# Kernel tuning notes

Hardware: AMD Instinct MI355X
Metric: run time of the kernel (lower is better)

The kernel has to match this reference:

```python
import jax, jax.numpy as jnp
import numpy as np

B, S, D, H = 8, 1024, 1024, 16
DK = D // H  # 64


def setup_inputs() -> dict:
    key = jax.random.key(0)
    ks = jax.random.split(key, 12)
    def w(k):
        return (jax.random.normal(k, (D, D), dtype=jnp.float32) * 0.02)
    def b(k):
        return (jax.random.normal(k, (D,), dtype=jnp.float32) * 0.02)
    return {
        "q": jax.random.normal(ks[0], (B, S, D), dtype=jnp.float32),
        "k": jax.random.normal(ks[1], (B, S, D), dtype=jnp.float32),
        "v": jax.random.normal(ks[2], (B, S, D), dtype=jnp.float32),
        "mask": jax.random.randint(ks[3], (B, 1, S, S), 0, 2, dtype=jnp.int32),
        "WQ_w": w(ks[4]), "WQ_b": b(ks[5]),
        "WK_w": w(ks[6]), "WK_b": b(ks[7]),
        "WV_w": w(ks[8]), "WV_b": b(ks[9]),
        "WO_w": w(ks[10]), "WO_b": b(ks[11]),
    }


def reference(q, k, v, mask, WQ_w, WQ_b, WK_w, WK_b, WV_w, WV_b, WO_w, WO_b):
    # nn.Linear: y = x @ W.T + b
    Q = (q @ WQ_w.T + WQ_b).reshape(B, S, H, DK)
    K = (k @ WK_w.T + WK_b).reshape(B, S, H, DK)
    V = (v @ WV_w.T + WV_b).reshape(B, S, H, DK)
    # scores: [B, H, Sq, Sk]
    scores = jnp.einsum("bqhd,bkhd->bhqk", Q, K) / jnp.sqrt(jnp.float32(DK))
    scores = jnp.where(mask == 0, jnp.float32(-1e9), scores)
    attn = jax.nn.softmax(scores, axis=-1)
    # dropout p=0.0 -> identity
    out = jnp.einsum("bhqk,bkhd->bqhd", attn, V).reshape(B, S, D)
    return out @ WO_w.T + WO_b
```

## Files before the change

kernel.cpp:

```cpp
#include <hip/hip_runtime.h>
#include <math.h>

typedef __bf16 bf16;
typedef __bf16 bf16x8 __attribute__((ext_vector_type(8)));
typedef __bf16 bf16x4 __attribute__((ext_vector_type(4)));
typedef float f32x4 __attribute__((ext_vector_type(4)));

constexpr int B_ = 8, S_ = 1024, D_ = 1024, H_ = 16, DK_ = 64;
constexpr int M_ = B_ * S_;
constexpr size_t A8 = (size_t)1 << 23;
constexpr size_t W1 = (size_t)1 << 20;
constexpr float QSCALE = 0.18033688011112042f;

#if __has_builtin(__builtin_amdgcn_exp2f)
#define EXP2F(x) __builtin_amdgcn_exp2f(x)
#else
#define EXP2F(x) exp2f(x)
#endif
#if __has_builtin(__builtin_amdgcn_rcpf)
#define RCPF(x) __builtin_amdgcn_rcpf(x)
#else
#define RCPF(x) (1.0f / (x))
#endif

#define GAS(p) ((const __attribute__((address_space(1))) void*)(p))
#define LAS(p) ((__attribute__((address_space(3))) void*)(p))

template<int CTRL>
__device__ __forceinline__ float row_ror(float v) {
    int i = __builtin_bit_cast(int, v);
    i = __builtin_amdgcn_update_dpp(i, i, CTRL, 0xF, 0xF, false);
    return __builtin_bit_cast(float, i);
}
__device__ __forceinline__ float rowmax16(float v) {
    v = fmaxf(v, row_ror<0x121>(v));
    v = fmaxf(v, row_ror<0x122>(v));
    v = fmaxf(v, row_ror<0x124>(v));
    v = fmaxf(v, row_ror<0x128>(v));
    return v;
}
__device__ __forceinline__ float rowsum16(float v) {
    v += row_ror<0x121>(v);
    v += row_ror<0x122>(v);
    v += row_ror<0x124>(v);
    v += row_ror<0x128>(v);
    return v;
}

__global__ __launch_bounds__(256) void cvt_all(
    const float* __restrict__ q, const float* __restrict__ k,
    const float* __restrict__ v, const float* __restrict__ w0,
    const float* __restrict__ w1, const float* __restrict__ w2,
    const float* __restrict__ w3, bf16* __restrict__ dst)
{
    size_t e = ((size_t)blockIdx.x * 256 + threadIdx.x) * 8;
    const float* src;
    size_t off;
    if (e < 3 * A8) {
        int t = (int)(e >> 23);
        src = (t == 0) ? q : (t == 1) ? k : v;
        off = e & (A8 - 1);
    } else {
        size_t ew = e - 3 * A8;
        int t = (int)(ew >> 20);
        src = (t == 0) ? w0 : (t == 1) ? w1 : (t == 2) ? w2 : w3;
        off = ew & (W1 - 1);
    }
    float4 a = *(const float4*)(src + off);
    float4 b = *(const float4*)(src + off + 4);
    bf16x8 o = { (bf16)a.x, (bf16)a.y, (bf16)a.z, (bf16)a.w,
                 (bf16)b.x, (bf16)b.y, (bf16)b.z, (bf16)b.w };
    *(bf16x8*)(dst + e) = o;
}

__global__ __launch_bounds__(256) void mask_cvt(
    const int* __restrict__ mask, bf16* __restrict__ mp)
{
    const int bx = blockIdx.x;
    const int kt = bx & 15, qt = (bx >> 4) & 15, b = bx >> 8;
    const int tid = threadIdx.x;
    const int w = tid >> 6, lane = tid & 63;
    const int quad = lane >> 4, l15 = lane & 15;

    const int* src = mask + ((size_t)b << 20)
                   + (size_t)(qt * 64 + w * 16 + quad * 4) * 1024
                   + kt * 64 + l15;
    bf16 vals[16];
#pragma unroll
    for (int j = 0; j < 4; ++j)
#pragma unroll
        for (int r = 0; r < 4; ++r) {
            int m = src[(size_t)r * 1024 + j * 16];
            vals[j * 4 + r] = m ? (bf16)0.0f : (bf16)(-1e9f);
        }
    bf16* dst = mp + (((size_t)(b * 16 + qt) * 16 + kt) << 12) + (w * 64 + lane) * 16;
    bf16x8 o0 = { vals[0], vals[1], vals[2],  vals[3],  vals[4],  vals[5],  vals[6],  vals[7]  };
    bf16x8 o1 = { vals[8], vals[9], vals[10], vals[11], vals[12], vals[13], vals[14], vals[15] };
    *(bf16x8*)dst = o0;
    *(bf16x8*)(dst + 8) = o1;
}

template<int OUT_MODE>
__global__ __launch_bounds__(256) void gemm_mfma(
    const bf16* __restrict__ X, const bf16* __restrict__ W,
    const float* __restrict__ bias, void* __restrict__ outv, float oscale)
{
    constexpr int K = 1024;
    __shared__ bf16 As[128 * 32];
    __shared__ bf16 Bs[128 * 32];

    const int tid  = threadIdx.x;
    const int lane = tid & 63;
    const int w    = tid >> 6;
    const int wm   = w & 1, wn = w >> 1;
    const int quad = lane >> 4, l15 = lane & 15;
    const int bm = blockIdx.x * 128, bn = blockIdx.y * 128;

    f32x4 acc[4][4];
#pragma unroll
    for (int i = 0; i < 4; ++i)
#pragma unroll
        for (int j = 0; j < 4; ++j)
#pragma unroll
            for (int r = 0; r < 4; ++r) acc[i][j][r] = 0.f;

    const int lrow = lane >> 2;
    const int lcol = (lane & 3) * 8;

    for (int k0 = 0; k0 < K; k0 += 32) {
        __syncthreads();
#pragma unroll
        for (int i = 0; i < 2; ++i) {
            const int rbase = w * 16 + i * 64;
            __builtin_amdgcn_global_load_lds(
                GAS(X + (size_t)(bm + rbase + lrow) * K + k0 + lcol),
                LAS(As + rbase * 32), 16, 0, 0);
            __builtin_amdgcn_global_load_lds(
                GAS(W + (size_t)(bn + rbase + lrow) * K + k0 + lcol),
                LAS(Bs + rbase * 32), 16, 0, 0);
        }
        __syncthreads();

        bf16x8 a[4], b[4];
#pragma unroll
        for (int i = 0; i < 4; ++i)
            a[i] = *(const bf16x8*)(As + (wm * 64 + i * 16 + l15) * 32 + quad * 8);
#pragma unroll
        for (int j = 0; j < 4; ++j)
            b[j] = *(const bf16x8*)(Bs + (wn * 64 + j * 16 + l15) * 32 + quad * 8);
#pragma unroll
        for (int i = 0; i < 4; ++i)
#pragma unroll
            for (int j = 0; j < 4; ++j)
                acc[i][j] = __builtin_amdgcn_mfma_f32_16x16x32_bf16(
                    a[i], b[j], acc[i][j], 0, 0, 0);
    }

#pragma unroll
    for (int i = 0; i < 4; ++i) {
#pragma unroll
        for (int j = 0; j < 4; ++j) {
            const int n = bn + wn * 64 + j * 16 + l15;
            const float bs = bias[n];
            if (OUT_MODE == 2) {
                const int m0 = bm + wm * 64 + i * 16 + quad * 4;
                const int bb = m0 >> 10, s0 = m0 & 1023;
                const int h = n >> 6, dk = n & 63;
                bf16x4 o;
#pragma unroll
                for (int r = 0; r < 4; ++r) o[r] = (bf16)(acc[i][j][r] + bs);
                *(bf16x4*)((bf16*)outv + (((size_t)(bb * 16 + h) * 64 + dk) << 10) + s0) = o;
            } else {
#pragma unroll
                for (int r = 0; r < 4; ++r) {
                    const int m = bm + wm * 64 + i * 16 + quad * 4 + r;
                    const float val = acc[i][j][r] + bs;
                    if (OUT_MODE == 0) {
                        ((float*)outv)[(size_t)m * 1024 + n] = val;
                    } else {
                        const int bb = m >> 10, s = m & 1023;
                        const int h = n >> 6, dk = n & 63;
                        ((bf16*)outv)[(((size_t)(bb * 16 + h)) * 1024 + s) * 64 + dk] =
                            (bf16)(val * oscale);
                    }
                }
            }
        }
    }
}

#define LDT 72
#define LDP 64

__global__ __launch_bounds__(256) void attn_mfma(
    const bf16* __restrict__ Q, const bf16* __restrict__ Kt,
    const bf16* __restrict__ Vt, const bf16* __restrict__ maskp,
    bf16* __restrict__ out)
{
    __shared__ bf16 smem[3 * 64 * LDT];
    bf16* Qs = smem;
    bf16* Ks = smem + 64 * LDT;
    bf16* Vs = smem + 2 * 64 * LDT;
    bf16* Ps = smem;

    const int tid  = threadIdx.x;
    const int lane = tid & 63;
    const int w    = tid >> 6;
    const int quad = lane >> 4, l15 = lane & 15;

    const int qt = blockIdx.x & 15;
    const int h  = (blockIdx.x >> 4) & 15;
    const int b  = blockIdx.x >> 8;

    const bf16* Qg  = Q  + ((size_t)(b * H_ + h) * S_ + qt * 64) * DK_;
    const bf16* Kg  = Kt + (size_t)(b * H_ + h) * S_ * DK_;
    const bf16* Vgt = Vt + ((size_t)(b * H_ + h) << 16);
    const bf16* mtb = maskp + (((size_t)(b * 16 + qt) * 16) << 12) + (w * 64 + lane) * 16;

    const int rr = tid >> 3;
    const int cc = (tid & 7) * 8;
    *(bf16x8*)(Qs + rr * LDT + cc)        = *(const bf16x8*)(Qg + rr * 64 + cc);
    *(bf16x8*)(Qs + (rr + 32) * LDT + cc) = *(const bf16x8*)(Qg + (rr + 32) * 64 + cc);
    __syncthreads();

    bf16x8 qa[2];
#pragma unroll
    for (int t = 0; t < 2; ++t)
        qa[t] = *(const bf16x8*)(Qs + (w * 16 + l15) * LDT + t * 32 + quad * 8);

    f32x4 O[4];
#pragma unroll
    for (int dj = 0; dj < 4; ++dj)
#pragma unroll
        for (int r = 0; r < 4; ++r) O[dj][r] = 0.f;
    float mrow[4] = { -INFINITY, -INFINITY, -INFINITY, -INFINITY };
    float lrow[4] = { 0.f, 0.f, 0.f, 0.f };

    const int pswz = quad << 4;
    const int rswz = (l15 >> 2) << 4;
    bf16* PsW = Ps + (w * 16 + quad * 4) * LDP;
    const bf16* PsR = Ps + (w * 16 + l15) * LDP;

    for (int kt = 0; kt < 16; ++kt) {
        __syncthreads();
        bf16x8 k0 = *(const bf16x8*)(Kg + kt * 4096 + rr * 64 + cc);
        bf16x8 k1 = *(const bf16x8*)(Kg + kt * 4096 + (rr + 32) * 64 + cc);
        bf16x8 v0 = *(const bf16x8*)(Vgt + (size_t)rr * 1024 + kt * 64 + cc);
        bf16x8 v1 = *(const bf16x8*)(Vgt + (size_t)(rr + 32) * 1024 + kt * 64 + cc);
        bf16x8 mv0 = *(const bf16x8*)(mtb + ((size_t)kt << 12));
        bf16x8 mv1 = *(const bf16x8*)(mtb + ((size_t)kt << 12) + 8);
        *(bf16x8*)(Ks + rr * LDT + cc)        = k0;
        *(bf16x8*)(Ks + (rr + 32) * LDT + cc) = k1;
        *(bf16x8*)(Vs + rr * LDT + cc)        = v0;
        *(bf16x8*)(Vs + (rr + 32) * LDT + cc) = v1;
        __syncthreads();

        f32x4 sf[4];
#pragma unroll
        for (int j = 0; j < 4; ++j)
#pragma unroll
            for (int r = 0; r < 4; ++r) sf[j][r] = 0.f;
#pragma unroll
        for (int t = 0; t < 2; ++t) {
#pragma unroll
            for (int j = 0; j < 4; ++j) {
                bf16x8 kb = *(const bf16x8*)(Ks + (j * 16 + l15) * LDT + t * 32 + quad * 8);
                sf[j] = __builtin_amdgcn_mfma_f32_16x16x32_bf16(qa[t], kb, sf[j], 0, 0, 0);
            }
        }

#pragma unroll
        for (int j = 0; j < 4; ++j)
#pragma unroll
            for (int r = 0; r < 4; ++r)
                sf[j][r] += (float)((j < 2 ? mv0 : mv1)[(j & 1) * 4 + r]);

        float tmax[4];
#pragma unroll
        for (int r = 0; r < 4; ++r)
            tmax[r] = rowmax16(fmaxf(fmaxf(sf[0][r], sf[1][r]), fmaxf(sf[2][r], sf[3][r])));

        float alpha[4], psum[4];
#pragma unroll
        for (int r = 0; r < 4; ++r) {
            const float mn = fmaxf(mrow[r], tmax[r]);
            alpha[r] = EXP2F(mrow[r] - mn);
            mrow[r] = mn;
            psum[r] = 0.f;
        }
#pragma unroll
        for (int j = 0; j < 4; ++j)
#pragma unroll
            for (int r = 0; r < 4; ++r) {
                const float p = EXP2F(sf[j][r] - mrow[r]);
                const bf16 pb = (bf16)p;
                PsW[r * LDP + ((j * 16 + l15) ^ pswz)] = pb;
                psum[r] += (float)pb;
            }
#pragma unroll
        for (int r = 0; r < 4; ++r) {
            psum[r] = rowsum16(psum[r]);
            lrow[r] = lrow[r] * alpha[r] + psum[r];
        }
#pragma unroll
        for (int dj = 0; dj < 4; ++dj)
#pragma unroll
            for (int r = 0; r < 4; ++r) O[dj][r] *= alpha[r];

#pragma unroll
        for (int t = 0; t < 2; ++t) {
            bf16x8 pa = *(const bf16x8*)(PsR + ((t * 32 + quad * 8) ^ rswz));
#pragma unroll
            for (int dj = 0; dj < 4; ++dj) {
                bf16x8 vb = *(const bf16x8*)(Vs + (dj * 16 + l15) * LDT + t * 32 + quad * 8);
                O[dj] = __builtin_amdgcn_mfma_f32_16x16x32_bf16(pa, vb, O[dj], 0, 0, 0);
            }
        }
    }

    float rinv[4];
#pragma unroll
    for (int r = 0; r < 4; ++r) rinv[r] = RCPF(lrow[r]);
#pragma unroll
    for (int dj = 0; dj < 4; ++dj)
#pragma unroll
        for (int r = 0; r < 4; ++r)
            out[((size_t)b * S_ + qt * 64 + w * 16 + quad * 4 + r) * D_
                + h * DK_ + dj * 16 + l15] = (bf16)(O[dj][r] * rinv[r]);
}

extern "C" void kernel_launch(void* const* d_in, const int* in_sizes, int n_in,
                              void* d_out, int out_size, void* d_ws, size_t ws_size,
                              hipStream_t stream) {
    const float* q    = (const float*)d_in[0];
    const float* k    = (const float*)d_in[1];
    const float* v    = (const float*)d_in[2];
    const int*   mask = (const int*)d_in[3];
    const float* WQw  = (const float*)d_in[4];
    const float* WQb  = (const float*)d_in[5];
    const float* WKw  = (const float*)d_in[6];
    const float* WKb  = (const float*)d_in[7];
    const float* WVw  = (const float*)d_in[8];
    const float* WVb  = (const float*)d_in[9];
    const float* WOw  = (const float*)d_in[10];
    const float* WOb  = (const float*)d_in[11];

    bf16* ws = (bf16*)d_ws;
    bf16* qb  = ws;
    bf16* kb  = qb + A8;
    bf16* vb  = kb + A8;
    bf16* wqb = vb + A8;
    bf16* wkb = wqb + W1;
    bf16* wvb = wkb + W1;
    bf16* wob = wvb + W1;
    bf16* Qp  = wob + W1;
    bf16* Kp  = Qp + A8;
    bf16* Vp  = Kp + A8;
    bf16* maskp = qb;
    bf16* AO    = kb;

    cvt_all<<<dim3(14336), 256, 0, stream>>>(q, k, v, WQw, WKw, WVw, WOw, ws);

    dim3 gg(M_ / 128, D_ / 128);
    gemm_mfma<1><<<gg, 256, 0, stream>>>(qb, wqb, WQb, (void*)Qp, QSCALE);
    gemm_mfma<1><<<gg, 256, 0, stream>>>(kb, wkb, WKb, (void*)Kp, 1.0f);
    gemm_mfma<2><<<gg, 256, 0, stream>>>(vb, wvb, WVb, (void*)Vp, 1.0f);

    mask_cvt<<<dim3(2048), 256, 0, stream>>>(mask, maskp);

    attn_mfma<<<dim3(2048), 256, 0, stream>>>(Qp, Kp, Vp, maskp, AO);

    gemm_mfma<0><<<gg, 256, 0, stream>>>(AO, wob, WOb, d_out, 1.0f);
}
```

Before: 387.9 us.

## Rewrite attention with 32x32 MFMA, async double-buffered K/V, lazy rescale

The attention kernel now gives each wave 32 query rows, computing S^T = K·Q^T and O^T = V^T·P^T with 32x32x16 MFMAs. P stays in registers and is exchanged through ds_bpermute, so the LDS round trip for P goes away. K/V tiles are double-buffered in swizzled LDS via global_load_lds. The mask is stored as fp32 in an accumulator-ready layout and used as the initial accumulator, and max rescaling is skipped unless the row max grows by more than a threshold. This is meant to cut LDS traffic, barriers and VALU work, at the cost of doubling the mask buffer size and more register pressure.

```diff
diff --git a/kernel.cpp b/kernel.cpp
--- a/kernel.cpp
+++ b/kernel.cpp
@@ -5,6 +5,8 @@
 typedef __bf16 bf16x8 __attribute__((ext_vector_type(8)));
 typedef __bf16 bf16x4 __attribute__((ext_vector_type(4)));
 typedef float f32x4 __attribute__((ext_vector_type(4)));
+typedef float f32x16 __attribute__((ext_vector_type(16)));
+typedef int i32x4 __attribute__((ext_vector_type(4)));
 
 constexpr int B_ = 8, S_ = 1024, D_ = 1024, H_ = 16, DK_ = 64;
 constexpr int M_ = B_ * S_;
@@ -26,26 +28,19 @@
 #define GAS(p) ((const __attribute__((address_space(1))) void*)(p))
 #define LAS(p) ((__attribute__((address_space(3))) void*)(p))
 
-template<int CTRL>
-__device__ __forceinline__ float row_ror(float v) {
-    int i = __builtin_bit_cast(int, v);
-    i = __builtin_amdgcn_update_dpp(i, i, CTRL, 0xF, 0xF, false);
-    return __builtin_bit_cast(float, i);
-}
-__device__ __forceinline__ float rowmax16(float v) {
-    v = fmaxf(v, row_ror<0x121>(v));
-    v = fmaxf(v, row_ror<0x122>(v));
-    v = fmaxf(v, row_ror<0x124>(v));
-    v = fmaxf(v, row_ror<0x128>(v));
-    return v;
-}
-__device__ __forceinline__ float rowsum16(float v) {
-    v += row_ror<0x121>(v);
-    v += row_ror<0x122>(v);
-    v += row_ror<0x124>(v);
-    v += row_ror<0x128>(v);
-    return v;
-}
+__device__ __forceinline__ float xor32f(float v, int bpidx) {
+    return __builtin_bit_cast(float,
+        __builtin_amdgcn_ds_bpermute(bpidx, __builtin_bit_cast(int, v)));
+}
+__device__ __forceinline__ int xor32i(int v, int bpidx) {
+    return __builtin_amdgcn_ds_bpermute(bpidx, v);
+}
+__device__ __forceinline__ int pack_bf16(bf16 lo, bf16 hi) {
+    return (int)(unsigned)__builtin_bit_cast(unsigned short, lo)
+         | ((int)(unsigned)__builtin_bit_cast(unsigned short, hi) << 16);
+}
+
+struct F4Q { f32x4 a, b, c, d; };
 
 __global__ __launch_bounds__(256) void cvt_all(
     const float* __restrict__ q, const float* __restrict__ k,
@@ -74,30 +69,26 @@
 }
 
 __global__ __launch_bounds__(256) void mask_cvt(
-    const int* __restrict__ mask, bf16* __restrict__ mp)
+    const int* __restrict__ mask, float* __restrict__ mf)
 {
     const int bx = blockIdx.x;
-    const int kt = bx & 15, qt = (bx >> 4) & 15, b = bx >> 8;
+    const int kt = bx & 15, qt = (bx >> 4) & 7, b = bx >> 7;
     const int tid = threadIdx.x;
     const int w = tid >> 6, lane = tid & 63;
-    const int quad = lane >> 4, l15 = lane & 15;
-
-    const int* src = mask + ((size_t)b << 20)
-                   + (size_t)(qt * 64 + w * 16 + quad * 4) * 1024
-                   + kt * 64 + l15;
-    bf16 vals[16];
-#pragma unroll
-    for (int j = 0; j < 4; ++j)
-#pragma unroll
-        for (int r = 0; r < 4; ++r) {
-            int m = src[(size_t)r * 1024 + j * 16];
-            vals[j * 4 + r] = m ? (bf16)0.0f : (bf16)(-1e9f);
-        }
-    bf16* dst = mp + (((size_t)(b * 16 + qt) * 16 + kt) << 12) + (w * 64 + lane) * 16;
-    bf16x8 o0 = { vals[0], vals[1], vals[2],  vals[3],  vals[4],  vals[5],  vals[6],  vals[7]  };
-    bf16x8 o1 = { vals[8], vals[9], vals[10], vals[11], vals[12], vals[13], vals[14], vals[15] };
-    *(bf16x8*)dst = o0;
-    *(bf16x8*)(dst + 8) = o1;
+    const int hi = lane >> 5, l31 = lane & 31;
+    const int q = qt * 128 + w * 32 + l31;
+
+    const int* src = mask + ((size_t)b << 20) + (size_t)q * 1024 + kt * 64 + hi * 4;
+    float* dst = mf + (size_t)bx * 8192 + w * 2048 + lane * 4;
+#pragma unroll
+    for (int blk = 0; blk < 2; ++blk)
+#pragma unroll
+        for (int rr = 0; rr < 4; ++rr) {
+            int4 m = *(const int4*)(src + blk * 32 + rr * 8);
+            f32x4 o = { m.x ? 0.f : -1e9f, m.y ? 0.f : -1e9f,
+                        m.z ? 0.f : -1e9f, m.w ? 0.f : -1e9f };
+            *(f32x4*)(dst + (blk * 4 + rr) * 256) = o;
+        }
 }
 
 template<int OUT_MODE>
@@ -189,144 +180,158 @@
     }
 }
 
-#define LDT 72
-#define LDP 64
-
 __global__ __launch_bounds__(256) void attn_mfma(
     const bf16* __restrict__ Q, const bf16* __restrict__ Kt,
-    const bf16* __restrict__ Vt, const bf16* __restrict__ maskp,
+    const bf16* __restrict__ Vt, const float* __restrict__ mf,
     bf16* __restrict__ out)
 {
-    __shared__ bf16 smem[3 * 64 * LDT];
-    bf16* Qs = smem;
-    bf16* Ks = smem + 64 * LDT;
-    bf16* Vs = smem + 2 * 64 * LDT;
-    bf16* Ps = smem;
+    __shared__ bf16 smem[2 * 2 * 4096];
 
     const int tid  = threadIdx.x;
     const int lane = tid & 63;
     const int w    = tid >> 6;
-    const int quad = lane >> 4, l15 = lane & 15;
-
-    const int qt = blockIdx.x & 15;
-    const int h  = (blockIdx.x >> 4) & 15;
-    const int b  = blockIdx.x >> 8;
-
-    const bf16* Qg  = Q  + ((size_t)(b * H_ + h) * S_ + qt * 64) * DK_;
-    const bf16* Kg  = Kt + (size_t)(b * H_ + h) * S_ * DK_;
-    const bf16* Vgt = Vt + ((size_t)(b * H_ + h) << 16);
-    const bf16* mtb = maskp + (((size_t)(b * 16 + qt) * 16) << 12) + (w * 64 + lane) * 16;
-
-    const int rr = tid >> 3;
-    const int cc = (tid & 7) * 8;
-    *(bf16x8*)(Qs + rr * LDT + cc)        = *(const bf16x8*)(Qg + rr * 64 + cc);
-    *(bf16x8*)(Qs + (rr + 32) * LDT + cc) = *(const bf16x8*)(Qg + (rr + 32) * 64 + cc);
+    const int hi   = lane >> 5, l31 = lane & 31;
+
+    const int wid = (blockIdx.x & 7) * 128 + (blockIdx.x >> 3);
+    const int qt = wid & 7;
+    const int h  = (wid >> 3) & 15;
+    const int b  = wid >> 7;
+
+    const bf16* Qg  = Q + ((size_t)((b * H_ + h) * S_) + qt * 128 + w * 32) * DK_;
+    const char* Kgh = (const char*)(Kt + (size_t)(b * H_ + h) * S_ * DK_);
+    const char* Vgh = (const char*)(Vt + ((size_t)(b * H_ + h) << 16));
+    const float* mtb = mf + (size_t)((b * 8 + qt) * 16) * 8192 + w * 2048 + lane * 4;
+
+    const int tA = tid,        rA = tA >> 3, cA = (tA & 7) * 16;
+    const int tB = 256 + tid,  rB = tB >> 3, cB = (tB & 7) * 16;
+    const int kSrcA = rA * 128  + (cA ^ ((rA & 7) << 4));
+    const int kSrcB = rB * 128  + (cB ^ ((rB & 7) << 4));
+    const int vSrcA = rA * 2048 + (cA ^ ((rA & 7) << 4));
+    const int vSrcB = rB * 2048 + (cB ^ ((rB & 7) << 4));
+
+    auto stage = [&](int buf, int tkt) {
+        bf16* Ks = smem + buf * 8192;
+        bf16* Vs = Ks + 4096;
+        const char* kg = Kgh + (size_t)tkt * 8192;
+        const char* vg = Vgh + (size_t)tkt * 128;
+        __builtin_amdgcn_global_load_lds(GAS(kg + kSrcA), LAS(Ks + w * 512),        16, 0, 0);
+        __builtin_amdgcn_global_load_lds(GAS(kg + kSrcB), LAS(Ks + 2048 + w * 512), 16, 0, 0);
+        __builtin_amdgcn_global_load_lds(GAS(vg + vSrcA), LAS(Vs + w * 512),        16, 0, 0);
+        __builtin_amdgcn_global_load_lds(GAS(vg + vSrcB), LAS(Vs + 2048 + w * 512), 16, 0, 0);
+    };
+
+    stage(0, 0);
+
+    bf16x8 qf[4];
+#pragma unroll
+    for (int ks = 0; ks < 4; ++ks)
+        qf[ks] = *(const bf16x8*)(Qg + (size_t)l31 * 64 + ks * 16 + hi * 8);
+
+    f32x16 O0, O1;
+#pragma unroll
+    for (int r = 0; r < 16; ++r) { O0[r] = 0.f; O1[r] = 0.f; }
+    float mrow = -INFINITY, lrowv = 0.f;
+    const int bpidx = (lane ^ 32) << 2;
+    const int swz = (l31 & 7) << 4;
+
     __syncthreads();
 
-    bf16x8 qa[2];
-#pragma unroll
-    for (int t = 0; t < 2; ++t)
-        qa[t] = *(const bf16x8*)(Qs + (w * 16 + l15) * LDT + t * 32 + quad * 8);
-
-    f32x4 O[4];
-#pragma unroll
-    for (int dj = 0; dj < 4; ++dj)
-#pragma unroll
-        for (int r = 0; r < 4; ++r) O[dj][r] = 0.f;
-    float mrow[4] = { -INFINITY, -INFINITY, -INFINITY, -INFINITY };
-    float lrow[4] = { 0.f, 0.f, 0.f, 0.f };
-
-    const int pswz = quad << 4;
-    const int rswz = (l15 >> 2) << 4;
-    bf16* PsW = Ps + (w * 16 + quad * 4) * LDP;
-    const bf16* PsR = Ps + (w * 16 + l15) * LDP;
-
+#pragma unroll 1
     for (int kt = 0; kt < 16; ++kt) {
+        const int buf = kt & 1;
+        const bf16* Ks = smem + buf * 8192;
+        const bf16* Vs = Ks + 4096;
+        const char* KsB = (const char*)Ks;
+        const char* VsB = (const char*)Vs;
+        const float* mk = mtb + (size_t)kt * 8192;
+
+        F4Q mq0 = { *(const f32x4*)(mk + 0),    *(const f32x4*)(mk + 256),
+                    *(const f32x4*)(mk + 512),  *(const f32x4*)(mk + 768) };
+        F4Q mq1 = { *(const f32x4*)(mk + 1024), *(const f32x4*)(mk + 1280),
+                    *(const f32x4*)(mk + 1536), *(const f32x4*)(mk + 1792) };
+        f32x16 acc0 = __builtin_bit_cast(f32x16, mq0);
+        f32x16 acc1 = __builtin_bit_cast(f32x16, mq1);
+
+        if (kt + 1 < 16) stage(buf ^ 1, kt + 1);
+
+#pragma unroll
+        for (int ks = 0; ks < 4; ++ks) {
+            const int cb = ks * 32 + hi * 16;
+            bf16x8 k0 = *(const bf16x8*)(KsB + l31 * 128        + (cb ^ swz));
+            bf16x8 k1 = *(const bf16x8*)(KsB + (l31 + 32) * 128 + (cb ^ swz));
+            acc0 = __builtin_amdgcn_mfma_f32_32x32x16_bf16(k0, qf[ks], acc0, 0, 0, 0);
+            acc1 = __builtin_amdgcn_mfma_f32_32x32x16_bf16(k1, qf[ks], acc1, 0, 0, 0);
+        }
+
+        float red[8];
+#pragma unroll
+        for (int i = 0; i < 8; ++i)
+            red[i] = fmaxf(fmaxf(acc0[i], acc0[i + 8]), fmaxf(acc1[i], acc1[i + 8]));
+#pragma unroll
+        for (int i = 0; i < 4; ++i) red[i] = fmaxf(red[i], red[i + 4]);
+        float mx = fmaxf(fmaxf(red[0], red[1]), fmaxf(red[2], red[3]));
+        mx = fmaxf(mx, xor32f(mx, bpidx));
+
+        if (__any(mx > mrow + 8.0f)) {
+            const float mn = fmaxf(mrow, mx);
+            const float alpha = EXP2F(mrow - mn);
+            mrow = mn;
+            lrowv *= alpha;
+#pragma unroll
+            for (int r = 0; r < 16; ++r) { O0[r] *= alpha; O1[r] *= alpha; }
+        }
+
+#pragma unroll
+        for (int r = 0; r < 16; ++r) acc0[r] = EXP2F(acc0[r] - mrow);
+#pragma unroll
+        for (int r = 0; r < 16; ++r) acc1[r] = EXP2F(acc1[r] - mrow);
+
+        int wd0[8], wd1[8];
+        float ps = 0.f;
+#pragma unroll
+        for (int s = 0; s < 8; ++s) {
+            bf16 e0 = (bf16)acc0[2 * s], o0 = (bf16)acc0[2 * s + 1];
+            bf16 e1 = (bf16)acc1[2 * s], o1 = (bf16)acc1[2 * s + 1];
+            ps += (float)e0 + (float)o0 + (float)e1 + (float)o1;
+            wd0[s] = pack_bf16(e0, o0);
+            wd1[s] = pack_bf16(e1, o1);
+        }
+        ps += xor32f(ps, bpidx);
+        lrowv += ps;
+
+#pragma unroll
+        for (int ks = 0; ks < 4; ++ks) {
+            const int s0 = (ks & 1) * 4;
+            int p0, p1, p2, p3;
+            if (ks < 2) { p0 = wd0[s0]; p1 = wd0[s0 + 1]; p2 = wd0[s0 + 2]; p3 = wd0[s0 + 3]; }
+            else        { p0 = wd1[s0]; p1 = wd1[s0 + 1]; p2 = wd1[s0 + 2]; p3 = wd1[s0 + 3]; }
+            const int q0 = xor32i(p0, bpidx);
+            const int q1 = xor32i(p1, bpidx);
+            const int q2 = xor32i(p2, bpidx);
+            const int q3 = xor32i(p3, bpidx);
+            i32x4 pw = { hi ? q2 : p0, hi ? q3 : p1, hi ? p2 : q0, hi ? p3 : q1 };
+            bf16x8 pa = __builtin_bit_cast(bf16x8, pw);
+
+            const int cb = ks * 32 + hi * 16;
+            bf16x8 v0 = *(const bf16x8*)(VsB + l31 * 128        + (cb ^ swz));
+            bf16x8 v1 = *(const bf16x8*)(VsB + (l31 + 32) * 128 + (cb ^ swz));
+            O0 = __builtin_amdgcn_mfma_f32_32x32x16_bf16(v0, pa, O0, 0, 0, 0);
+            O1 = __builtin_amdgcn_mfma_f32_32x32x16_bf16(v1, pa, O1, 0, 0, 0);
+        }
         __syncthreads();
-        bf16x8 k0 = *(const bf16x8*)(Kg + kt * 4096 + rr * 64 + cc);
-        bf16x8 k1 = *(const bf16x8*)(Kg + kt * 4096 + (rr + 32) * 64 + cc);
-        bf16x8 v0 = *(const bf16x8*)(Vgt + (size_t)rr * 1024 + kt * 64 + cc);
-        bf16x8 v1 = *(const bf16x8*)(Vgt + (size_t)(rr + 32) * 1024 + kt * 64 + cc);
-        bf16x8 mv0 = *(const bf16x8*)(mtb + ((size_t)kt << 12));
-        bf16x8 mv1 = *(const bf16x8*)(mtb + ((size_t)kt << 12) + 8);
-        *(bf16x8*)(Ks + rr * LDT + cc)        = k0;
-        *(bf16x8*)(Ks + (rr + 32) * LDT + cc) = k1;
-        *(bf16x8*)(Vs + rr * LDT + cc)        = v0;
-        *(bf16x8*)(Vs + (rr + 32) * LDT + cc) = v1;
-        __syncthreads();
-
-        f32x4 sf[4];
-#pragma unroll
-        for (int j = 0; j < 4; ++j)
-#pragma unroll
-            for (int r = 0; r < 4; ++r) sf[j][r] = 0.f;
-#pragma unroll
-        for (int t = 0; t < 2; ++t) {
-#pragma unroll
-            for (int j = 0; j < 4; ++j) {
-                bf16x8 kb = *(const bf16x8*)(Ks + (j * 16 + l15) * LDT + t * 32 + quad * 8);
-                sf[j] = __builtin_amdgcn_mfma_f32_16x16x32_bf16(qa[t], kb, sf[j], 0, 0, 0);
-            }
-        }
-
-#pragma unroll
-        for (int j = 0; j < 4; ++j)
-#pragma unroll
-            for (int r = 0; r < 4; ++r)
-                sf[j][r] += (float)((j < 2 ? mv0 : mv1)[(j & 1) * 4 + r]);
-
-        float tmax[4];
-#pragma unroll
-        for (int r = 0; r < 4; ++r)
-            tmax[r] = rowmax16(fmaxf(fmaxf(sf[0][r], sf[1][r]), fmaxf(sf[2][r], sf[3][r])));
-
-        float alpha[4], psum[4];
-#pragma unroll
-        for (int r = 0; r < 4; ++r) {
-            const float mn = fmaxf(mrow[r], tmax[r]);
-            alpha[r] = EXP2F(mrow[r] - mn);
-            mrow[r] = mn;
-            psum[r] = 0.f;
-        }
-#pragma unroll
-        for (int j = 0; j < 4; ++j)
-#pragma unroll
-            for (int r = 0; r < 4; ++r) {
-                const float p = EXP2F(sf[j][r] - mrow[r]);
-                const bf16 pb = (bf16)p;
-                PsW[r * LDP + ((j * 16 + l15) ^ pswz)] = pb;
-                psum[r] += (float)pb;
-            }
-#pragma unroll
-        for (int r = 0; r < 4; ++r) {
-            psum[r] = rowsum16(psum[r]);
-            lrow[r] = lrow[r] * alpha[r] + psum[r];
-        }
-#pragma unroll
-        for (int dj = 0; dj < 4; ++dj)
-#pragma unroll
-            for (int r = 0; r < 4; ++r) O[dj][r] *= alpha[r];
-
-#pragma unroll
-        for (int t = 0; t < 2; ++t) {
-            bf16x8 pa = *(const bf16x8*)(PsR + ((t * 32 + quad * 8) ^ rswz));
-#pragma unroll
-            for (int dj = 0; dj < 4; ++dj) {
-                bf16x8 vb = *(const bf16x8*)(Vs + (dj * 16 + l15) * LDT + t * 32 + quad * 8);
-                O[dj] = __builtin_amdgcn_mfma_f32_16x16x32_bf16(pa, vb, O[dj], 0, 0, 0);
-            }
-        }
-    }
-
-    float rinv[4];
-#pragma unroll
-    for (int r = 0; r < 4; ++r) rinv[r] = RCPF(lrow[r]);
-#pragma unroll
-    for (int dj = 0; dj < 4; ++dj)
-#pragma unroll
-        for (int r = 0; r < 4; ++r)
-            out[((size_t)b * S_ + qt * 64 + w * 16 + quad * 4 + r) * D_
-                + h * DK_ + dj * 16 + l15] = (bf16)(O[dj][r] * rinv[r]);
+    }
+
+    const float rinv = RCPF(lrowv);
+    bf16* og = out + ((size_t)b * S_ + qt * 128 + w * 32 + l31) * D_ + h * DK_;
+#pragma unroll
+    for (int rr = 0; rr < 4; ++rr) {
+        bf16x4 o0 = { (bf16)(O0[rr * 4 + 0] * rinv), (bf16)(O0[rr * 4 + 1] * rinv),
+                      (bf16)(O0[rr * 4 + 2] * rinv), (bf16)(O0[rr * 4 + 3] * rinv) };
+        bf16x4 o1 = { (bf16)(O1[rr * 4 + 0] * rinv), (bf16)(O1[rr * 4 + 1] * rinv),
+                      (bf16)(O1[rr * 4 + 2] * rinv), (bf16)(O1[rr * 4 + 3] * rinv) };
+        *(bf16x4*)(og + rr * 8 + hi * 4)      = o0;
+        *(bf16x4*)(og + 32 + rr * 8 + hi * 4) = o1;
+    }
 }
 
 extern "C" void kernel_launch(void* const* d_in, const int* in_sizes, int n_in,
@@ -356,8 +361,8 @@
     bf16* Qp  = wob + W1;
     bf16* Kp  = Qp + A8;
     bf16* Vp  = Kp + A8;
-    bf16* maskp = qb;
-    bf16* AO    = kb;
+    float* maskf = (float*)qb;
+    bf16* AO     = vb;
 
     cvt_all<<<dim3(14336), 256, 0, stream>>>(q, k, v, WQw, WKw, WVw, WOw, ws);
 
@@ -366,9 +371,9 @@
     gemm_mfma<1><<<gg, 256, 0, stream>>>(kb, wkb, WKb, (void*)Kp, 1.0f);
     gemm_mfma<2><<<gg, 256, 0, stream>>>(vb, wvb, WVb, (void*)Vp, 1.0f);
 
-    mask_cvt<<<dim3(2048), 256, 0, stream>>>(mask, maskp);
-
-    attn_mfma<<<dim3(2048), 256, 0, stream>>>(Qp, Kp, Vp, maskp, AO);
+    mask_cvt<<<dim3(1024), 256, 0, stream>>>(mask, maskf);
+
+    attn_mfma<<<dim3(1024), 256, 0, stream>>>(Qp, Kp, Vp, maskf, AO);
 
     gemm_mfma<0><<<gg, 256, 0, stream>>>(AO, wob, WOb, d_out, 1.0f);
 }
```

Result: faster. 367.2 us (-5.3%).
